# Kernel tuning notes

Measured on AMD Instinct MI355X. Metric: run time of the kernel, lower is better.

## Reference

```python
import jax, jax.numpy as jnp
import numpy as np

B, N = 1, 768
C_S, C_P = 384, 128
K = 32            # relpos_k
NBIN = 2 * K + 1  # 65
EPS = 1e-10


def setup_inputs() -> dict:
    key = jax.random.key(0)
    ks = jax.random.split(key, 8)
    s = jax.random.normal(ks[0], (B, N, C_S), jnp.float32)
    trans = jax.random.normal(ks[1], (B, N, 3), jnp.float32)
    p_mask = jnp.ones((B, N, N), jnp.float32)
    # Linear params (torch default: U(-1/sqrt(fan_in), 1/sqrt(fan_in)))
    def lin(k, out_f, in_f):
        k1, k2 = jax.random.split(k)
        bound = 1.0 / np.sqrt(in_f)
        W = jax.random.uniform(k1, (out_f, in_f), jnp.float32, -bound, bound)
        b = jax.random.uniform(k2, (out_f,), jnp.float32, -bound, bound)
        return W, b
    W_i, b_i = lin(ks[2], C_P, C_S)
    W_j, b_j = lin(ks[3], C_P, C_S)
    W_rel, b_rel = lin(ks[4], C_P, NBIN)
    W_t, b_t = lin(ks[5], C_P, 1)
    return {"s": s, "trans": trans, "p_mask": p_mask,
            "W_i": W_i, "b_i": b_i, "W_j": W_j, "b_j": b_j,
            "W_rel": W_rel, "b_rel": b_rel, "W_t": W_t, "b_t": b_t}


def reference(s, trans, p_mask, W_i, b_i, W_j, b_j, W_rel, b_rel, W_t, b_t):
    # p_i + p_j broadcast sum: [B,N,1,c_p] + [B,1,N,c_p]
    p_i = jnp.einsum('bnc,pc->bnp', s, W_i) + b_i   # [B,N,c_p]
    p_j = jnp.einsum('bnc,pc->bnp', s, W_j) + b_j
    p = p_i[:, :, None, :] + p_j[:, None, :, :]      # [B,N,N,c_p]

    # relpos: r[:, :, None] - r[:, None, :] with r = arange(N) (same every batch).
    # argmin_|d - v| over v = [-K..K] with integer d has a unique minimizer == clip(d,-K,K),
    # and one_hot(b) @ W_rel.T == W_rel.T[b]  (direct gather, same math).
    r = jnp.arange(N)
    bins = jnp.clip(r[:, None] - r[None, :], -K, K) + K  # [N,N] in [0, NBIN)
    rel = jnp.take(W_rel.T, bins, axis=0) + b_rel        # [N,N,c_p]
    p = p + rel[None]

    # template v1: pairwise distance of trans, then Linear(1 -> c_p)
    diff = trans[:, :, None, :] - trans[:, None, :, :]   # [B,N,N,3]
    dist = jnp.sqrt(EPS + jnp.sum(diff * diff, axis=-1)) # [B,N,N]
    p = p + dist[..., None] * W_t[:, 0] + b_t            # Linear(1->c_p)

    p = p * p_mask[..., None]
    return p
```

## Files before the change

### kernel.cpp

```cpp
#include <hip/hip_runtime.h>
#include <math.h>

#define N 768
#define CS 384
#define CP 128
#define NBIN 65

__global__ __launch_bounds__(256) void proj_kernel(
    const float* __restrict__ s,
    const float* __restrict__ Wi, const float* __restrict__ bi,
    const float* __restrict__ Wj, const float* __restrict__ bj,
    float* __restrict__ pI, float* __restrict__ pJ) {
  __shared__ float s_sh[4 * CS];
  const int n0 = blockIdx.x * 4;
  const int tid = threadIdx.x;
  for (int i = tid; i < 4 * CS; i += 256)
    s_sh[i] = s[n0 * CS + i];
  __syncthreads();

  const int which = tid >> 7;
  const int p = tid & 127;
  const float* W = which ? Wj : Wi;
  const float b = which ? bj[p] : bi[p];
  const float4* W4 = reinterpret_cast<const float4*>(W + p * CS);
  const float4* S4 = reinterpret_cast<const float4*>(s_sh);

  float acc0 = b, acc1 = b, acc2 = b, acc3 = b;
  for (int c4 = 0; c4 < CS / 4; ++c4) {
    const float4 w = W4[c4];
    const float4 s0 = S4[0 * (CS / 4) + c4];
    const float4 s1 = S4[1 * (CS / 4) + c4];
    const float4 s2 = S4[2 * (CS / 4) + c4];
    const float4 s3 = S4[3 * (CS / 4) + c4];
    acc0 += s0.x * w.x + s0.y * w.y + s0.z * w.z + s0.w * w.w;
    acc1 += s1.x * w.x + s1.y * w.y + s1.z * w.z + s1.w * w.w;
    acc2 += s2.x * w.x + s2.y * w.y + s2.z * w.z + s2.w * w.w;
    acc3 += s3.x * w.x + s3.y * w.y + s3.z * w.z + s3.w * w.w;
  }
  float* outp = which ? pJ : pI;
  outp[(n0 + 0) * CP + p] = acc0;
  outp[(n0 + 1) * CP + p] = acc1;
  outp[(n0 + 2) * CP + p] = acc2;
  outp[(n0 + 3) * CP + p] = acc3;
}

__global__ void rel_kernel(const float* __restrict__ Wrel,
                           const float* __restrict__ brel,
                           const float* __restrict__ bt,
                           float* __restrict__ relT) {
  const int b = blockIdx.x;
  const int p = threadIdx.x;
  relT[b * CP + p] = Wrel[p * NBIN + b] + brel[p] + bt[p];
}

__global__ __launch_bounds__(256) void pair_kernel(
    const float* __restrict__ pI, const float* __restrict__ pJ,
    const float* __restrict__ relT, const float* __restrict__ Wt,
    const float* __restrict__ trans, const float* __restrict__ mask,
    float* __restrict__ out) {
  const int n = blockIdx.y;
  const int pair = threadIdx.x >> 5;
  const int v = threadIdx.x & 31;
  const int m = blockIdx.x * 8 + pair;

  const float4 pi4 = reinterpret_cast<const float4*>(pI)[n * (CP / 4) + v];
  const float4 pj4 = reinterpret_cast<const float4*>(pJ)[m * (CP / 4) + v];
  int d = n - m;
  d = d < -32 ? -32 : (d > 32 ? 32 : d);
  const float4 rel4 = reinterpret_cast<const float4*>(relT)[(d + 32) * (CP / 4) + v];
  const float4 wt4 = reinterpret_cast<const float4*>(Wt)[v];
  const float msk = mask[n * N + m];

  const float dx = trans[n * 3 + 0] - trans[m * 3 + 0];
  const float dy = trans[n * 3 + 1] - trans[m * 3 + 1];
  const float dz = trans[n * 3 + 2] - trans[m * 3 + 2];
  const float dist = sqrtf(1e-10f + dx * dx + dy * dy + dz * dz);

  float4 o;
  o.x = (pi4.x + pj4.x + rel4.x + dist * wt4.x) * msk;
  o.y = (pi4.y + pj4.y + rel4.y + dist * wt4.y) * msk;
  o.z = (pi4.z + pj4.z + rel4.z + dist * wt4.z) * msk;
  o.w = (pi4.w + pj4.w + rel4.w + dist * wt4.w) * msk;

  reinterpret_cast<float4*>(out)[(size_t)(n * N + m) * (CP / 4) + v] = o;
}

extern "C" void kernel_launch(void* const* d_in, const int* in_sizes, int n_in,
                              void* d_out, int out_size, void* d_ws, size_t ws_size,
                              hipStream_t stream) {
  const float* s      = (const float*)d_in[0];
  const float* trans  = (const float*)d_in[1];
  const float* p_mask = (const float*)d_in[2];
  const float* Wi     = (const float*)d_in[3];
  const float* bi     = (const float*)d_in[4];
  const float* Wj     = (const float*)d_in[5];
  const float* bj     = (const float*)d_in[6];
  const float* Wrel   = (const float*)d_in[7];
  const float* brel   = (const float*)d_in[8];
  const float* Wt     = (const float*)d_in[9];
  const float* bt     = (const float*)d_in[10];
  float* out = (float*)d_out;

  float* ws   = (float*)d_ws;
  float* pI   = ws;
  float* pJ   = ws + N * CP;
  float* relT = ws + 2 * N * CP;

  proj_kernel<<<N / 4, 256, 0, stream>>>(s, Wi, bi, Wj, bj, pI, pJ);
  rel_kernel<<<NBIN, CP, 0, stream>>>(Wrel, brel, bt, relT);
  pair_kernel<<<dim3(N / 8, N), 256, 0, stream>>>(pI, pJ, relT, Wt, trans, p_mask, out);
}
```

Before: 83.82 us.

## Merge prep kernels, tile pair kernel over 64 columns with nontemporal stores

```diff
diff --git a/kernel.cpp b/kernel.cpp
--- a/kernel.cpp
+++ b/kernel.cpp
@@ -5,15 +5,29 @@
 #define CS 384
 #define CP 128
 #define NBIN 65
+#define MT 64
 
-__global__ __launch_bounds__(256) void proj_kernel(
+typedef float f4 __attribute__((ext_vector_type(4)));
+
+__global__ __launch_bounds__(256) void prep_kernel(
     const float* __restrict__ s,
     const float* __restrict__ Wi, const float* __restrict__ bi,
     const float* __restrict__ Wj, const float* __restrict__ bj,
-    float* __restrict__ pI, float* __restrict__ pJ) {
+    const float* __restrict__ Wrel, const float* __restrict__ brel,
+    const float* __restrict__ bt,
+    float* __restrict__ pI, float* __restrict__ pJ, float* __restrict__ relT) {
+  const int tid = threadIdx.x;
+
+  if (blockIdx.x >= N / 4) {
+    const int bb = (blockIdx.x - N / 4) * 2 + (tid >> 7);
+    const int p = tid & 127;
+    if (bb < NBIN)
+      relT[bb * CP + p] = Wrel[p * NBIN + bb] + brel[p] + bt[p];
+    return;
+  }
+
   __shared__ float s_sh[4 * CS];
   const int n0 = blockIdx.x * 4;
-  const int tid = threadIdx.x;
   for (int i = tid; i < 4 * CS; i += 256)
     s_sh[i] = s[n0 * CS + i];
   __syncthreads();
@@ -22,16 +36,16 @@
   const int p = tid & 127;
   const float* W = which ? Wj : Wi;
   const float b = which ? bj[p] : bi[p];
-  const float4* W4 = reinterpret_cast<const float4*>(W + p * CS);
-  const float4* S4 = reinterpret_cast<const float4*>(s_sh);
+  const f4* W4 = reinterpret_cast<const f4*>(W + p * CS);
+  const f4* S4 = reinterpret_cast<const f4*>(s_sh);
 
   float acc0 = b, acc1 = b, acc2 = b, acc3 = b;
   for (int c4 = 0; c4 < CS / 4; ++c4) {
-    const float4 w = W4[c4];
-    const float4 s0 = S4[0 * (CS / 4) + c4];
-    const float4 s1 = S4[1 * (CS / 4) + c4];
-    const float4 s2 = S4[2 * (CS / 4) + c4];
-    const float4 s3 = S4[3 * (CS / 4) + c4];
+    const f4 w = W4[c4];
+    const f4 s0 = S4[0 * (CS / 4) + c4];
+    const f4 s1 = S4[1 * (CS / 4) + c4];
+    const f4 s2 = S4[2 * (CS / 4) + c4];
+    const f4 s3 = S4[3 * (CS / 4) + c4];
     acc0 += s0.x * w.x + s0.y * w.y + s0.z * w.z + s0.w * w.w;
     acc1 += s1.x * w.x + s1.y * w.y + s1.z * w.z + s1.w * w.w;
     acc2 += s2.x * w.x + s2.y * w.y + s2.z * w.z + s2.w * w.w;
@@ -44,45 +58,57 @@
   outp[(n0 + 3) * CP + p] = acc3;
 }
 
-__global__ void rel_kernel(const float* __restrict__ Wrel,
-                           const float* __restrict__ brel,
-                           const float* __restrict__ bt,
-                           float* __restrict__ relT) {
-  const int b = blockIdx.x;
-  const int p = threadIdx.x;
-  relT[b * CP + p] = Wrel[p * NBIN + b] + brel[p] + bt[p];
-}
-
 __global__ __launch_bounds__(256) void pair_kernel(
     const float* __restrict__ pI, const float* __restrict__ pJ,
     const float* __restrict__ relT, const float* __restrict__ Wt,
     const float* __restrict__ trans, const float* __restrict__ mask,
     float* __restrict__ out) {
+  __shared__ float dist_sh[MT];
+  __shared__ float msk_sh[MT];
+
   const int n = blockIdx.y;
-  const int pair = threadIdx.x >> 5;
-  const int v = threadIdx.x & 31;
-  const int m = blockIdx.x * 8 + pair;
+  const int m0 = blockIdx.x * MT;
+  const int tid = threadIdx.x;
 
-  const float4 pi4 = reinterpret_cast<const float4*>(pI)[n * (CP / 4) + v];
-  const float4 pj4 = reinterpret_cast<const float4*>(pJ)[m * (CP / 4) + v];
-  int d = n - m;
-  d = d < -32 ? -32 : (d > 32 ? 32 : d);
-  const float4 rel4 = reinterpret_cast<const float4*>(relT)[(d + 32) * (CP / 4) + v];
-  const float4 wt4 = reinterpret_cast<const float4*>(Wt)[v];
-  const float msk = mask[n * N + m];
+  if (tid < MT) {
+    const int m = m0 + tid;
+    const float dx = trans[n * 3 + 0] - trans[m * 3 + 0];
+    const float dy = trans[n * 3 + 1] - trans[m * 3 + 1];
+    const float dz = trans[n * 3 + 2] - trans[m * 3 + 2];
+    dist_sh[tid] = sqrtf(1e-10f + dx * dx + dy * dy + dz * dz);
+    msk_sh[tid] = mask[n * N + m];
+  }
+  __syncthreads();
 
-  const float dx = trans[n * 3 + 0] - trans[m * 3 + 0];
-  const float dy = trans[n * 3 + 1] - trans[m * 3 + 1];
-  const float dz = trans[n * 3 + 2] - trans[m * 3 + 2];
-  const float dist = sqrtf(1e-10f + dx * dx + dy * dy + dz * dz);
+  const int v = tid & 31;
+  const int slot = tid >> 5;
 
-  float4 o;
-  o.x = (pi4.x + pj4.x + rel4.x + dist * wt4.x) * msk;
-  o.y = (pi4.y + pj4.y + rel4.y + dist * wt4.y) * msk;
-  o.z = (pi4.z + pj4.z + rel4.z + dist * wt4.z) * msk;
-  o.w = (pi4.w + pj4.w + rel4.w + dist * wt4.w) * msk;
+  const f4 pi4 = reinterpret_cast<const f4*>(pI)[n * (CP / 4) + v];
+  const f4 wt4 = reinterpret_cast<const f4*>(Wt)[v];
+  const f4* __restrict__ pJ4 = reinterpret_cast<const f4*>(pJ);
+  const f4* __restrict__ rel4 = reinterpret_cast<const f4*>(relT);
+  f4* __restrict__ out4 = reinterpret_cast<f4*>(out) + ((size_t)n * N + m0) * (CP / 4);
 
-  reinterpret_cast<float4*>(out)[(size_t)(n * N + m) * (CP / 4) + v] = o;
+#pragma unroll
+  for (int k = 0; k < MT / 8; ++k) {
+    const int mi = k * 8 + slot;
+    const int m = m0 + mi;
+    int d = n - m;
+    d = d < -32 ? -32 : (d > 32 ? 32 : d);
+
+    const f4 pj4 = pJ4[m * (CP / 4) + v];
+    const f4 rl = rel4[(d + 32) * (CP / 4) + v];
+    const float dist = dist_sh[mi];
+    const float msk = msk_sh[mi];
+
+    f4 o;
+    o.x = (pi4.x + pj4.x + rl.x + dist * wt4.x) * msk;
+    o.y = (pi4.y + pj4.y + rl.y + dist * wt4.y) * msk;
+    o.z = (pi4.z + pj4.z + rl.z + dist * wt4.z) * msk;
+    o.w = (pi4.w + pj4.w + rl.w + dist * wt4.w) * msk;
+
+    __builtin_nontemporal_store(o, &out4[mi * (CP / 4) + v]);
+  }
 }
 
 extern "C" void kernel_launch(void* const* d_in, const int* in_sizes, int n_in,
@@ -106,7 +132,8 @@
   float* pJ   = ws + N * CP;
   float* relT = ws + 2 * N * CP;
 
-  proj_kernel<<<N / 4, 256, 0, stream>>>(s, Wi, bi, Wj, bj, pI, pJ);
-  rel_kernel<<<NBIN, CP, 0, stream>>>(Wrel, brel, bt, relT);
-  pair_kernel<<<dim3(N / 8, N), 256, 0, stream>>>(pI, pJ, relT, Wt, trans, p_mask, out);
+  prep_kernel<<<N / 4 + (NBIN + 1) / 2, 256, 0, stream>>>(
+      s, Wi, bi, Wj, bj, Wrel, brel, bt, pI, pJ, relT);
+  pair_kernel<<<dim3(N / MT, N), 256, 0, stream>>>(
+      pI, pJ, relT, Wt, trans, p_mask, out);
 }
```

New measurement: 75.31 us. 1.11x faster.
